# Performance work log

Measured on AMD Instinct MI355X. Metric: run time of the kernel, lower is better.

The kernel has to match this reference:

```python
import jax, jax.numpy as jnp
import numpy as np

B, C, H, W = 4, 64, 64, 64
RC, RS = 8, 4  # channel reduction, spatial reduction
CR = C // RC
KS = 2 * RS - 1  # 7


def _conv(x, w, b, stride, pad):
    y = jax.lax.conv_general_dilated(
        x, w, (stride, stride), [(pad, pad), (pad, pad)],
        dimension_numbers=('NCHW', 'OIHW', 'NCHW'))
    return y + b[None, :, None, None]


def setup_inputs() -> dict:
    key = jax.random.key(0)
    ks = jax.random.split(key, 13)

    def w_init(k, shape):
        fan_in = shape[1] * shape[2] * shape[3]
        return jax.random.normal(k, shape, jnp.float32) / jnp.sqrt(fan_in)

    x = jax.random.normal(ks[0], (B, C, H, W), jnp.float32)
    return {
        'x': x,
        'w1': w_init(ks[1], (CR, C, 1, 1)), 'b1': jnp.zeros((CR,), jnp.float32),
        'w2': w_init(ks[2], (CR, C, 1, 1)), 'b2': jnp.zeros((CR,), jnp.float32),
        'w3': w_init(ks[3], (C, C, 1, 1)),  'b3': jnp.zeros((C,), jnp.float32),
        'w4': w_init(ks[4], (C, C, KS, KS)), 'b4': jnp.zeros((C,), jnp.float32),
        'w5': w_init(ks[5], (C, C, KS, KS)), 'b5': jnp.zeros((C,), jnp.float32),
        'w6': w_init(ks[6], (C, C, 1, 1)),  'b6': jnp.zeros((C,), jnp.float32),
    }


def reference(x, w1, b1, w2, b2, w3, b3, w4, b4, w5, b5, w6, b6):
    gamma = 1.0
    x_ori = x
    b, c, h, w = x.shape
    n = h * w

    # ---- Block 1: spatial self-attention (SAGAN-style), N x N scores ----
    f = _conv(x, w1, b1, 1, 0).reshape(b, CR, n)   # [B, C/8, N]
    g = _conv(x, w2, b2, 1, 0).reshape(b, CR, n)   # [B, C/8, N]
    hh = _conv(x, w3, b3, 1, 0).reshape(b, c, n)   # [B, C, N]
    s = jnp.einsum('bci,bcj->bij', f, g)           # [B, N, N] = f^T g
    beta = jax.nn.softmax(s, axis=1)               # softmax over dim 1 (as in torch)
    o = jnp.einsum('bcn,bnm->bcm', hh, beta)       # [B, C, N]
    x2 = o.reshape(b, c, h, w)

    # ---- Block 2: channel attention over strided-conv features, C x C scores ----
    hp, wp = h // RS, w // RS
    npix = hp * wp
    f2 = _conv(x2, w4, b4, RS, RS - 1).reshape(b, c, npix)  # [B, C, N']
    g2 = _conv(x2, w5, b5, RS, RS - 1).reshape(b, c, npix)  # [B, C, N']
    h2 = _conv(x2, w6, b6, 1, 0).reshape(b, c, n)           # [B, C, N]
    s2 = jnp.einsum('bcn,bdn->bcd', f2, g2)                 # [B, C, C] = f g^T
    beta2 = jax.nn.softmax(s2, axis=1)
    # o[b,d,n] = sum_c h2[b,c,n] * beta2[b,c,d]
    o2 = jnp.einsum('bcn,bcd->bdn', h2, beta2).reshape(b, c, h, w)

    return gamma * o2 + x_ori
```

## Files before the change

### kernel.cpp

```cpp
#include <hip/hip_runtime.h>
#include <math.h>

#define BB 4
#define CC 64
#define CRR 8
#define NN 4096

typedef __attribute__((ext_vector_type(8))) short bf16x8;
typedef __attribute__((ext_vector_type(4))) float f32x4;

__device__ inline float bf2f(ushort u) {
    union { uint i; float f; } v; v.i = (uint)u << 16; return v.f;
}
__device__ inline ushort f2bf(float f) {
    uint u = __builtin_bit_cast(uint, f);
    u = (u + 0x7FFFu + ((u >> 16) & 1u)) >> 16;
    return (ushort)u;
}
__device__ inline uint bfpack2(float a, float b) {
    uint ua = __builtin_bit_cast(uint, a);
    uint ub = __builtin_bit_cast(uint, b);
    ua = (ua + 0x7FFFu + ((ua >> 16) & 1u)) >> 16;
    ub = (ub + 0x7FFFu + ((ub >> 16) & 1u)) & 0xFFFF0000u;
    return ua | ub;
}
__device__ inline uint pkrtz(float a, float b) {
    return __builtin_amdgcn_perm(__builtin_bit_cast(uint, b),
                                 __builtin_bit_cast(uint, a), 0x07060302u);
}
__device__ inline float fexp2(float x) {
#if __has_builtin(__builtin_amdgcn_exp2f)
    return __builtin_amdgcn_exp2f(x);
#else
    float r; asm("v_exp_f32 %0, %1" : "=v"(r) : "v"(x)); return r;
#endif
}

#define X2P_B 313600

__global__ __launch_bounds__(256) void produce_fgh(
    const float* __restrict__ x,
    const float* __restrict__ w1, const float* __restrict__ b1,
    const float* __restrict__ w2, const float* __restrict__ b2,
    const float* __restrict__ w3, const float* __restrict__ b3,
    ushort* __restrict__ fT, ushort* __restrict__ gT, ushort* __restrict__ hhb)
{
    const float LOG2E = 1.4426950408889634f;
    int t = threadIdx.x;
    int b = blockIdx.x & 3;
    int n = ((blockIdx.x >> 2) << 6) + (t & 63);
    int og = __builtin_amdgcn_readfirstlane(t >> 6);

    const float* xb = x + ((size_t)b << 18) + n;
    float xv[64];
#pragma unroll
    for (int c = 0; c < 64; ++c) xv[c] = xb[(size_t)c << 12];

    if (og == 0) {
        ushort fo[8], go[8];
#pragma unroll
        for (int k = 0; k < 8; ++k) {
            float a1 = b1[k], a2 = b2[k];
#pragma unroll
            for (int c = 0; c < 64; ++c) {
                a1 = fmaf(w1[k * 64 + c], xv[c], a1);
                a2 = fmaf(w2[k * 64 + c], xv[c], a2);
            }
            fo[k] = f2bf(a1 * LOG2E); go[k] = f2bf(a2);
        }
        uint4 fq = make_uint4((uint)fo[0] | ((uint)fo[1] << 16),
                              (uint)fo[2] | ((uint)fo[3] << 16),
                              (uint)fo[4] | ((uint)fo[5] << 16),
                              (uint)fo[6] | ((uint)fo[7] << 16));
        uint4 gq = make_uint4((uint)go[0] | ((uint)go[1] << 16),
                              (uint)go[2] | ((uint)go[3] << 16),
                              (uint)go[4] | ((uint)go[5] << 16),
                              (uint)go[6] | ((uint)go[7] << 16));
        *(uint4*)&fT[((size_t)b << 15) + (size_t)n * 8] = fq;
        *(uint4*)&gT[((size_t)b << 15) + (size_t)n * 8] = gq;
#pragma unroll
        for (int k = 0; k < 4; ++k) {
            float a = b3[k];
#pragma unroll
            for (int c = 0; c < 64; ++c) a = fmaf(w3[k * 64 + c], xv[c], a);
            hhb[((size_t)b << 18) + ((size_t)k << 12) + n] = f2bf(a);
        }
    } else {
        int c0 = og * 20 - 16;
#pragma unroll
        for (int k = 0; k < 20; ++k) {
            float a = b3[c0 + k];
#pragma unroll
            for (int c = 0; c < 64; ++c) a = fmaf(w3[(c0 + k) * 64 + c], xv[c], a);
            hhb[((size_t)b << 18) + ((size_t)(c0 + k) << 12) + n] = f2bf(a);
        }
    }
}

__global__ __launch_bounds__(256) void wtz_kernel(
    const float* __restrict__ w4, const float* __restrict__ w5,
    const float* __restrict__ w6,
    ushort* __restrict__ Wt, ushort* __restrict__ w6b, ushort* __restrict__ x2p)
{
    int bid = blockIdx.x;
    int t = threadIdx.x;
    if (bid < 128) {
        int conv = bid >> 6, co = bid & 63;
        const float* W = conv ? w5 : w4;
        for (int i = t; i < 3136; i += 256) {
            int ci = i / 49, kk = i - ci * 49;
            Wt[(((size_t)(conv * 64 + co)) * 49 + kk) * 64 + ci] = f2bf(W[co * 3136 + i]);
        }
    } else if (bid == 128) {
#pragma unroll
        for (int k = 0; k < 16; ++k) {
            int i = k * 256 + t;
            w6b[i] = f2bf(w6[i]);
        }
    } else {
        int gid = (bid - 129) * 256 + t;
        if (gid >= 4 * 804) return;
        int b = gid / 804;
        int i = gid - b * 804;
        int py, px;
        if (i < 210) { py = i / 70; px = i - py * 70; }
        else if (i < 420) { int j = i - 210; int r = j / 70; py = 67 + r; px = j - r * 70; }
        else { int j = i - 420; int r = j / 6; py = 3 + r; int c = j - r * 6; px = c < 3 ? c : 64 + c; }
        ushort* p = x2p + (size_t)b * X2P_B + (size_t)(py * 70 + px) * 64;
        uint4 z = make_uint4(0, 0, 0, 0);
#pragma unroll
        for (int k = 0; k < 8; ++k) *(uint4*)(p + k * 8) = z;
    }
}

__global__ __launch_bounds__(1024) void attn_kernel(
    const ushort* __restrict__ fT, const ushort* __restrict__ gT,
    const ushort* __restrict__ hhb, const ushort* __restrict__ w6b,
    const float* __restrict__ b6,
    ushort* __restrict__ x2p, ushort* __restrict__ h2b)
{
    __shared__ __align__(16) char smem[98304];
    ushort* hhT = (ushort*)smem;
    ushort* PstB = (ushort*)(smem + 65536);
    float* Acc = (float*)smem;
    float* Lq  = (float*)(smem + 69632);
    ushort* x2s = (ushort*)(smem + 70656);

    int t = threadIdx.x;
    int q = t >> 8, tq = t & 255;
    int l = t & 63;
    int wq = tq >> 6;
    int w16 = t >> 6;
    int ml = l & 15, g = l >> 4;
    int b = blockIdx.x & 3;
    int mt = blockIdx.x >> 2;
    int m0 = mt << 6;
    int col = m0 + wq * 16 + ml;

    const ushort* fTb = fT + ((size_t)b << 15) + (size_t)q * 8192;
    const ushort* gTb = gT + ((size_t)b << 15);
    const ushort* hhB = hhb + ((size_t)b << 18) + (q << 10);

    const bf16x8 z8 = {0, 0, 0, 0, 0, 0, 0, 0};
    const f32x4 z4 = {0.f, 0.f, 0.f, 0.f};

    bf16x8 gfrag = *(const bf16x8*)(gTb + (size_t)col * 8);
    if (g != 0) gfrag = z8;

    int sc = tq >> 2, sp = tq & 3;
    const ushort* hrowBase = hhB + (size_t)sc * 4096 + sp * 16;
    int hdst = q * 8192 + sp * 1024 + sc * 8;

    uint4 h0 = *(const uint4*)(hrowBase);
    uint4 h1 = *(const uint4*)(hrowBase + 8);
    *(uint4*)&hhT[hdst] = h0;
    *(uint4*)&hhT[hdst + 512] = h1;
    bf16x8 afc[4];
#pragma unroll
    for (int s = 0; s < 4; ++s)
        afc[s] = *(const bf16x8*)(fTb + (size_t)(16 * s + ml) * 8);

    f32x4 acc[4] = {z4, z4, z4, z4};
    float rsum = 0.f;
    int swz = (ml & 7) << 4;
    char* pbase = (char*)PstB + w16 * 2048;
    __syncthreads();

    for (int nt = 0; nt < 16; ++nt) {
        int buf = nt & 1;
        bf16x8 afn[4];
        if (nt < 15) {
            int n0 = (nt + 1) << 6;
            h0 = *(const uint4*)(hrowBase + n0);
            h1 = *(const uint4*)(hrowBase + n0 + 8);
#pragma unroll
            for (int s = 0; s < 4; ++s)
                afn[s] = *(const bf16x8*)(fTb + (size_t)(n0 + 16 * s + ml) * 8);
        }

        f32x4 Sv[4];
#pragma unroll
        for (int s = 0; s < 4; ++s)
            Sv[s] = __builtin_amdgcn_mfma_f32_16x16x32_bf16(afc[s], gfrag, z4, 0, 0, 0);

        uint plo[4], phi[4];
#pragma unroll
        for (int s = 0; s < 4; ++s) {
            float p0 = fexp2(Sv[s][0]);
            float p1 = fexp2(Sv[s][1]);
            float p2 = fexp2(Sv[s][2]);
            float p3 = fexp2(Sv[s][3]);
            rsum += (p0 + p1) + (p2 + p3);
            plo[s] = pkrtz(p0, p1);
            phi[s] = pkrtz(p2, p3);
        }

#pragma unroll
        for (int s = 0; s < 4; ++s) {
            uint off = (uint)((ml * 128 + 32 * s + 8 * g) ^ swz);
            *(uint2*)(pbase + off) = make_uint2(plo[s], phi[s]);
        }

#pragma unroll
        for (int kk = 0; kk < 2; ++kk) {
            uint off = (uint)((ml * 128 + 64 * kk + 16 * g) ^ swz);
            bf16x8 pf = *(const bf16x8*)(pbase + off);
#pragma unroll
            for (int ct = 0; ct < 4; ++ct) {
                bf16x8 hf = *(const bf16x8*)&hhT[q * 8192 + buf * 4096 + (kk * 4 + g) * 512 + (16 * ct + ml) * 8];
                acc[ct] = __builtin_amdgcn_mfma_f32_16x16x32_bf16(hf, pf, acc[ct], 0, 0, 0);
            }
        }

        if (nt < 15) {
            int nb = (nt + 1) & 1;
            *(uint4*)&hhT[hdst + nb * 4096] = h0;
            *(uint4*)&hhT[hdst + nb * 4096 + 512] = h1;
#pragma unroll
            for (int s = 0; s < 4; ++s) afc[s] = afn[s];
        }
        __syncthreads();
    }

    rsum += __shfl_xor(rsum, 16);
    rsum += __shfl_xor(rsum, 32);

    {
        float* arow = Acc + q * 4352 + (wq * 16 + ml) * 68;
#pragma unroll
        for (int ct = 0; ct < 4; ++ct)
            *(f32x4*)(arow + 16 * ct + 4 * g) = acc[ct];
        if (g == 0) Lq[q * 64 + wq * 16 + ml] = rsum;
    }
    __syncthreads();

    {
        int m = t >> 4, c0 = (t & 15) << 2;
        float Ltot = Lq[m] + Lq[64 + m] + Lq[128 + m] + Lq[192 + m];
        float rL = 1.f / Ltot;
        f32x4 v0 = *(const f32x4*)(Acc + 0 * 4352 + m * 68 + c0);
        f32x4 v1 = *(const f32x4*)(Acc + 1 * 4352 + m * 68 + c0);
        f32x4 v2 = *(const f32x4*)(Acc + 2 * 4352 + m * 68 + c0);
        f32x4 v3 = *(const f32x4*)(Acc + 3 * 4352 + m * 68 + c0);
        f32x4 v;
#pragma unroll
        for (int r = 0; r < 4; ++r)
            v[r] = ((v0[r] + v1[r]) + (v2[r] + v3[r])) * rL;
        uint2 pk = make_uint2(bfpack2(v[0], v[1]), bfpack2(v[2], v[3]));
        int px = m + 3, py = mt + 3;
        *(uint2*)(x2p + (size_t)b * X2P_B + (size_t)(py * 70 + px) * 64 + c0) = pk;
        *(uint2*)(x2s + m * 72 + c0) = pk;
    }
    __syncthreads();

    {
        int dt = w16 & 3, mq = w16 >> 2;
        f32x4 hacc = z4;
#pragma unroll
        for (int kk = 0; kk < 2; ++kk) {
            bf16x8 xf = *(const bf16x8*)(x2s + (mq * 16 + ml) * 72 + 32 * kk + 8 * g);
            bf16x8 wf = *(const bf16x8*)(w6b + (size_t)(16 * dt + ml) * 64 + 32 * kk + 8 * g);
            hacc = __builtin_amdgcn_mfma_f32_16x16x32_bf16(wf, xf, hacc, 0, 0, 0);
        }
        ushort* h2row = h2b + ((size_t)b << 18) + (m0 + mq * 16 + ml);
#pragma unroll
        for (int r = 0; r < 4; ++r) {
            int d = 16 * dt + 4 * g + r;
            h2row[(size_t)d << 12] = f2bf(hacc[r] + b6[d]);
        }
    }
}

__global__ __launch_bounds__(256) void conv7_split_kernel(
    const ushort* __restrict__ x2p, const ushort* __restrict__ Wt,
    float* __restrict__ part)
{
    int t = threadIdx.x;
    int l = t & 63, w = t >> 6;
    int ml = l & 15, g = l >> 4;
    int lb = (blockIdx.x & 7) * 28 + (blockIdx.x >> 3);
    int bc = lb / 28;
    int idx = (lb % 28) * 4 + w;
    int ky = idx >> 4;
    int ct = (idx >> 2) & 3;
    int og = idx & 3;
    int conv = bc & 1, b = bc >> 1;

    int co0 = ct * 16;
    const ushort* wb = Wt + (size_t)conv * 200704
                     + (size_t)(co0 + ml) * 3136 + (size_t)(ky * 7) * 64 + g * 8;
    const ushort* xbase = x2p + (size_t)b * X2P_B + g * 8;

    int pixoff[4];
#pragma unroll
    for (int s = 0; s < 4; ++s) {
        int opix = og * 64 + s * 16 + ml;
        int oy = opix >> 4, ox = opix & 15;
        pixoff[s] = ((oy * 4 + ky) * 70 + ox * 4) * 64;
    }

    const f32x4 z4 = {0.f, 0.f, 0.f, 0.f};
    f32x4 acc[4] = {z4, z4, z4, z4};

#pragma unroll
    for (int kx = 0; kx < 7; ++kx) {
#pragma unroll
        for (int ci0 = 0; ci0 < 64; ci0 += 32) {
            bf16x8 av = *(const bf16x8*)(wb + kx * 64 + ci0);
#pragma unroll
            for (int s = 0; s < 4; ++s) {
                bf16x8 bv = *(const bf16x8*)(xbase + pixoff[s] + kx * 64 + ci0);
                acc[s] = __builtin_amdgcn_mfma_f32_16x16x32_bf16(av, bv, acc[s], 0, 0, 0);
            }
        }
    }

    float* pb = part + (size_t)(ky * 8 + bc) * 16384;
#pragma unroll
    for (int s = 0; s < 4; ++s) {
        int opix = og * 64 + s * 16 + ml;
#pragma unroll
        for (int r = 0; r < 4; ++r) {
            int co = co0 + 4 * g + r;
            pb[co * 256 + opix] = acc[s][r];
        }
    }
}

__global__ __launch_bounds__(256) void conv7_reduce_kernel(
    const float* __restrict__ part, const float* __restrict__ b4,
    const float* __restrict__ b5, float* __restrict__ f2, float* __restrict__ g2)
{
    int idx = (blockIdx.x * 256 + threadIdx.x) * 4;
    int bc = idx >> 14;
    int co = (idx >> 8) & 63;
    int conv = bc & 1, b = bc >> 1;
    int sub = idx & 16383;
    float4 s = make_float4(0.f, 0.f, 0.f, 0.f);
#pragma unroll
    for (int ky = 0; ky < 7; ++ky) {
        float4 v = *(const float4*)&part[(size_t)(ky * 8 + bc) * 16384 + sub];
        s.x += v.x; s.y += v.y; s.z += v.z; s.w += v.w;
    }
    float bias = (conv ? b5 : b4)[co];
    s.x += bias; s.y += bias; s.z += bias; s.w += bias;
    float* y = conv ? g2 : f2;
    *(float4*)&y[(size_t)b * 16384 + sub] = s;
}

__global__ __launch_bounds__(1024) void s2_softmax_kernel(
    const float* __restrict__ f2, const float* __restrict__ g2,
    float* __restrict__ beta2)
{
    __shared__ __align__(16) float g2t[4][64][68];
    __shared__ __align__(16) float s2f[64][68];
    __shared__ float red[6][64];
    int t = threadIdx.x;
    int b = blockIdx.x;
    int q = t >> 8, tq = t & 255;
    int nb = q * 64;

    {
        int n = tq & 63, c0 = tq >> 6;
#pragma unroll
        for (int k = 0; k < 16; ++k) {
            int cc = c0 * 16 + k;
            g2t[q][n][cc] = g2[((size_t)(b * 64 + cc) << 8) + nb + n];
        }
    }
    __syncthreads();

    int c = tq & 63, dq = tq >> 6, d0 = dq * 16;
    float acc[16];
#pragma unroll
    for (int k = 0; k < 16; ++k) acc[k] = 0.f;
    const float* frow = f2 + ((size_t)(b * 64 + c) << 8) + nb;
#pragma unroll 4
    for (int n = 0; n < 64; ++n) {
        float fv = frow[n];
#pragma unroll
        for (int jj = 0; jj < 4; ++jj) {
            float4 gv = *(const float4*)&g2t[q][n][d0 + jj * 4];
            acc[jj * 4 + 0] = fmaf(fv, gv.x, acc[jj * 4 + 0]);
            acc[jj * 4 + 1] = fmaf(fv, gv.y, acc[jj * 4 + 1]);
            acc[jj * 4 + 2] = fmaf(fv, gv.z, acc[jj * 4 + 2]);
            acc[jj * 4 + 3] = fmaf(fv, gv.w, acc[jj * 4 + 3]);
        }
    }
    __syncthreads();
    float* part = &g2t[0][0][0];
#pragma unroll
    for (int k = 0; k < 16; ++k) part[q * 4096 + c * 64 + d0 + k] = acc[k];
    __syncthreads();
    {
        int idx = t * 4;
        int cc = idx >> 6, dd = idx & 63;
        float4 s0 = *(const float4*)&part[cc * 64 + dd];
        float4 s1 = *(const float4*)&part[4096 + cc * 64 + dd];
        float4 s2v = *(const float4*)&part[8192 + cc * 64 + dd];
        float4 s3 = *(const float4*)&part[12288 + cc * 64 + dd];
        float4 s;
        s.x = (s0.x + s1.x) + (s2v.x + s3.x);
        s.y = (s0.y + s1.y) + (s2v.y + s3.y);
        s.z = (s0.z + s1.z) + (s2v.z + s3.z);
        s.w = (s0.w + s1.w) + (s2v.w + s3.w);
        *(float4*)&s2f[cc][dd] = s;
    }
    __syncthreads();
    if (t < 256) {
        int d = t & 63, cq = t >> 6;
        float mx = -3e38f;
#pragma unroll
        for (int k = 0; k < 16; ++k) mx = fmaxf(mx, s2f[cq * 16 + k][d]);
        red[cq][d] = mx;
    }
    __syncthreads();
    if (t < 64)
        red[4][t] = fmaxf(fmaxf(red[0][t], red[1][t]), fmaxf(red[2][t], red[3][t]));
    __syncthreads();
    if (t < 256) {
        int d = t & 63, cq = t >> 6;
        float mx = red[4][d];
        float s = 0.f;
#pragma unroll
        for (int k = 0; k < 16; ++k) s += __expf(s2f[cq * 16 + k][d] - mx);
        red[cq][d] = s;
    }
    __syncthreads();
    if (t < 64)
        red[5][t] = 1.f / ((red[0][t] + red[1][t]) + (red[2][t] + red[3][t]));
    __syncthreads();
    if (t < 256) {
        int d = t & 63, cq = t >> 6;
        float mx = red[4][d], r = red[5][d];
#pragma unroll
        for (int k = 0; k < 16; ++k) {
            int cc = cq * 16 + k;
            beta2[((size_t)b << 12) + cc * 64 + d] = __expf(s2f[cc][d] - mx) * r;
        }
    }
}

__global__ __launch_bounds__(256) void o2_residual_kernel(
    const ushort* __restrict__ h2b, const float* __restrict__ beta2,
    const float* __restrict__ x, float* __restrict__ out)
{
    __shared__ __align__(16) float b2s[64][64];
    __shared__ float h2s[64][65];
    int t = threadIdx.x;
    int b = blockIdx.x & 3;
    int n0 = (blockIdx.x >> 2) << 6;

    {
#pragma unroll
        for (int k = 0; k < 16; ++k) {
            int idx = k * 256 + t;
            b2s[idx >> 6][idx & 63] = beta2[((size_t)b << 12) + idx];
        }
        int n = t & 63; int c0 = t >> 6;
#pragma unroll
        for (int k = 0; k < 16; ++k) {
            int cc = c0 * 16 + k;
            h2s[cc][n] = bf2f(h2b[((size_t)(b * 64 + cc) << 12) + n0 + n]);
        }
    }
    __syncthreads();

    int n = t & 63, dg = t >> 6, d0 = dg * 16;
    float acc[16];
#pragma unroll
    for (int k = 0; k < 16; ++k) acc[k] = 0.f;

    for (int cc = 0; cc < 64; ++cc) {
        float hv = h2s[cc][n];
#pragma unroll
        for (int jj = 0; jj < 4; ++jj) {
            float4 bv = *reinterpret_cast<const float4*>(&b2s[cc][d0 + jj * 4]);
            acc[jj * 4 + 0] = fmaf(hv, bv.x, acc[jj * 4 + 0]);
            acc[jj * 4 + 1] = fmaf(hv, bv.y, acc[jj * 4 + 1]);
            acc[jj * 4 + 2] = fmaf(hv, bv.z, acc[jj * 4 + 2]);
            acc[jj * 4 + 3] = fmaf(hv, bv.w, acc[jj * 4 + 3]);
        }
    }
#pragma unroll
    for (int k = 0; k < 16; ++k) {
        int d = d0 + k;
        size_t o = ((size_t)(b * 64 + d) << 12) + n0 + n;
        out[o] = acc[k] + x[o];
    }
}

extern "C" void kernel_launch(void* const* d_in, const int* in_sizes, int n_in,
                              void* d_out, int out_size, void* d_ws, size_t ws_size,
                              hipStream_t stream)
{
    const float* x  = (const float*)d_in[0];
    const float* w1 = (const float*)d_in[1];
    const float* b1 = (const float*)d_in[2];
    const float* w2 = (const float*)d_in[3];
    const float* b2 = (const float*)d_in[4];
    const float* w3 = (const float*)d_in[5];
    const float* b3 = (const float*)d_in[6];
    const float* w4 = (const float*)d_in[7];
    const float* b4 = (const float*)d_in[8];
    const float* w5 = (const float*)d_in[9];
    const float* b5 = (const float*)d_in[10];
    const float* w6 = (const float*)d_in[11];
    const float* b6 = (const float*)d_in[12];
    float* out = (float*)d_out;

    ushort* u = (ushort*)d_ws;
    ushort* fT  = u;
    ushort* gT  = fT + 131072;
    ushort* hhb = gT + 131072;
    ushort* x2p = hhb + 1048576;
    ushort* h2b = x2p + 1254400;
    ushort* Wt  = h2b + 1048576;
    ushort* w6b = Wt + 401408;
    float* fr    = (float*)(w6b + 4096);
    float* f2    = fr;
    float* g2    = fr + 65536;
    float* beta2 = fr + 131072;
    float* part  = fr + 147456;

    produce_fgh<<<256, 256, 0, stream>>>(x, w1, b1, w2, b2, w3, b3, fT, gT, hhb);
    wtz_kernel<<<142, 256, 0, stream>>>(w4, w5, w6, Wt, w6b, x2p);
    attn_kernel<<<256, 1024, 0, stream>>>(fT, gT, hhb, w6b, b6, x2p, h2b);
    conv7_split_kernel<<<224, 256, 0, stream>>>(x2p, Wt, part);
    conv7_reduce_kernel<<<128, 256, 0, stream>>>(part, b4, b5, f2, g2);
    s2_softmax_kernel<<<BB, 1024, 0, stream>>>(f2, g2, beta2);
    o2_residual_kernel<<<256, 256, 0, stream>>>(h2b, beta2, x, out);
}
```

Measured before the change: 83.26 us.

## Pre-tile hh in MFMA fragment layout and read directly from global, drop LDS staging

The producer kernel now writes hh in a fragment-ready tiled layout (8 consecutive pixels per channel group), so the attention kernel can load MFMA B-operands straight from global/L2 instead of staging a transposed copy in LDS. This removes the LDS double-buffer, its stores, and the per-iteration __syncthreads in the main loop, and shrinks shared memory use. In exchange each wave issues more global loads per tile with no prefetch, so latency is exposed unless caches and occupancy hide it. The producer's hh stores become strided 2-byte scatters.

Result: slower. 86.77 us (+4.2%).

```diff
diff --git a/kernel.cpp b/kernel.cpp
--- a/kernel.cpp
+++ b/kernel.cpp
@@ -43,7 +43,7 @@
     const float* __restrict__ w1, const float* __restrict__ b1,
     const float* __restrict__ w2, const float* __restrict__ b2,
     const float* __restrict__ w3, const float* __restrict__ b3,
-    ushort* __restrict__ fT, ushort* __restrict__ gT, ushort* __restrict__ hhb)
+    ushort* __restrict__ fT, ushort* __restrict__ gT, ushort* __restrict__ hhf)
 {
     const float LOG2E = 1.4426950408889634f;
     int t = threadIdx.x;
@@ -55,6 +55,8 @@
     float xv[64];
 #pragma unroll
     for (int c = 0; c < 64; ++c) xv[c] = xb[(size_t)c << 12];
+
+    ushort* hn = hhf + ((size_t)b << 18) + ((size_t)(n >> 3) << 9) + (n & 7);
 
     if (og == 0) {
         ushort fo[8], go[8];
@@ -83,7 +85,7 @@
             float a = b3[k];
 #pragma unroll
             for (int c = 0; c < 64; ++c) a = fmaf(w3[k * 64 + c], xv[c], a);
-            hhb[((size_t)b << 18) + ((size_t)k << 12) + n] = f2bf(a);
+            hn[k << 3] = f2bf(a);
         }
     } else {
         int c0 = og * 20 - 16;
@@ -92,7 +94,7 @@
             float a = b3[c0 + k];
 #pragma unroll
             for (int c = 0; c < 64; ++c) a = fmaf(w3[(c0 + k) * 64 + c], xv[c], a);
-            hhb[((size_t)b << 18) + ((size_t)(c0 + k) << 12) + n] = f2bf(a);
+            hn[(c0 + k) << 3] = f2bf(a);
         }
     }
 }
@@ -135,13 +137,12 @@
 
 __global__ __launch_bounds__(1024) void attn_kernel(
     const ushort* __restrict__ fT, const ushort* __restrict__ gT,
-    const ushort* __restrict__ hhb, const ushort* __restrict__ w6b,
+    const ushort* __restrict__ hhf, const ushort* __restrict__ w6b,
     const float* __restrict__ b6,
     ushort* __restrict__ x2p, ushort* __restrict__ h2b)
 {
-    __shared__ __align__(16) char smem[98304];
-    ushort* hhT = (ushort*)smem;
-    ushort* PstB = (ushort*)(smem + 65536);
+    __shared__ __align__(16) char smem[79872];
+    ushort* PstB = (ushort*)smem;
     float* Acc = (float*)smem;
     float* Lq  = (float*)(smem + 69632);
     ushort* x2s = (ushort*)(smem + 70656);
@@ -159,7 +160,7 @@
 
     const ushort* fTb = fT + ((size_t)b << 15) + (size_t)q * 8192;
     const ushort* gTb = gT + ((size_t)b << 15);
-    const ushort* hhB = hhb + ((size_t)b << 18) + (q << 10);
+    const ushort* hhB = hhf + ((size_t)b << 18) + ((size_t)q << 16);
 
     const bf16x8 z8 = {0, 0, 0, 0, 0, 0, 0, 0};
     const f32x4 z4 = {0.f, 0.f, 0.f, 0.f};
@@ -167,14 +168,6 @@
     bf16x8 gfrag = *(const bf16x8*)(gTb + (size_t)col * 8);
     if (g != 0) gfrag = z8;
 
-    int sc = tq >> 2, sp = tq & 3;
-    const ushort* hrowBase = hhB + (size_t)sc * 4096 + sp * 16;
-    int hdst = q * 8192 + sp * 1024 + sc * 8;
-
-    uint4 h0 = *(const uint4*)(hrowBase);
-    uint4 h1 = *(const uint4*)(hrowBase + 8);
-    *(uint4*)&hhT[hdst] = h0;
-    *(uint4*)&hhT[hdst + 512] = h1;
     bf16x8 afc[4];
 #pragma unroll
     for (int s = 0; s < 4; ++s)
@@ -184,15 +177,11 @@
     float rsum = 0.f;
     int swz = (ml & 7) << 4;
     char* pbase = (char*)PstB + w16 * 2048;
-    __syncthreads();
 
     for (int nt = 0; nt < 16; ++nt) {
-        int buf = nt & 1;
         bf16x8 afn[4];
         if (nt < 15) {
             int n0 = (nt + 1) << 6;
-            h0 = *(const uint4*)(hrowBase + n0);
-            h1 = *(const uint4*)(hrowBase + n0 + 8);
 #pragma unroll
             for (int s = 0; s < 4; ++s)
                 afn[s] = *(const bf16x8*)(fTb + (size_t)(n0 + 16 * s + ml) * 8);
@@ -221,29 +210,28 @@
             *(uint2*)(pbase + off) = make_uint2(plo[s], phi[s]);
         }
 
+        const ushort* hnt = hhB + nt * 4096;
 #pragma unroll
         for (int kk = 0; kk < 2; ++kk) {
             uint off = (uint)((ml * 128 + 64 * kk + 16 * g) ^ swz);
             bf16x8 pf = *(const bf16x8*)(pbase + off);
 #pragma unroll
             for (int ct = 0; ct < 4; ++ct) {
-                bf16x8 hf = *(const bf16x8*)&hhT[q * 8192 + buf * 4096 + (kk * 4 + g) * 512 + (16 * ct + ml) * 8];
+                bf16x8 hf = *(const bf16x8*)(hnt + (kk * 4 + g) * 512 + (16 * ct + ml) * 8);
                 acc[ct] = __builtin_amdgcn_mfma_f32_16x16x32_bf16(hf, pf, acc[ct], 0, 0, 0);
             }
         }
 
         if (nt < 15) {
-            int nb = (nt + 1) & 1;
-            *(uint4*)&hhT[hdst + nb * 4096] = h0;
-            *(uint4*)&hhT[hdst + nb * 4096 + 512] = h1;
 #pragma unroll
             for (int s = 0; s < 4; ++s) afc[s] = afn[s];
         }
-        __syncthreads();
     }
 
     rsum += __shfl_xor(rsum, 16);
     rsum += __shfl_xor(rsum, 32);
+
+    __syncthreads();
 
     {
         float* arow = Acc + q * 4352 + (wq * 16 + ml) * 68;
@@ -532,8 +520,8 @@
     ushort* u = (ushort*)d_ws;
     ushort* fT  = u;
     ushort* gT  = fT + 131072;
-    ushort* hhb = gT + 131072;
-    ushort* x2p = hhb + 1048576;
+    ushort* hhf = gT + 131072;
+    ushort* x2p = hhf + 1048576;
     ushort* h2b = x2p + 1254400;
     ushort* Wt  = h2b + 1048576;
     ushort* w6b = Wt + 401408;
@@ -543,9 +531,9 @@
     float* beta2 = fr + 131072;
     float* part  = fr + 147456;
 
-    produce_fgh<<<256, 256, 0, stream>>>(x, w1, b1, w2, b2, w3, b3, fT, gT, hhb);
+    produce_fgh<<<256, 256, 0, stream>>>(x, w1, b1, w2, b2, w3, b3, fT, gT, hhf);
     wtz_kernel<<<142, 256, 0, stream>>>(w4, w5, w6, Wt, w6b, x2p);
-    attn_kernel<<<256, 1024, 0, stream>>>(fT, gT, hhb, w6b, b6, x2p, h2b);
+    attn_kernel<<<256, 1024, 0, stream>>>(fT, gT, hhf, w6b, b6, x2p, h2b);
     conv7_split_kernel<<<224, 256, 0, stream>>>(x2p, Wt, part);
     conv7_reduce_kernel<<<128, 256, 0, stream>>>(part, b4, b5, f2, g2);
     s2_softmax_kernel<<<BB, 1024, 0, stream>>>(f2, g2, beta2);
```

## Fuse strided 7x7 conv split-K partials and reduction into one kernel via LDS

Applied to the files above, without the earlier changes.

Merges the split-ky conv7 kernel and its separate reduction kernel into a single kernel. Each 448-thread block has seven waves, one per kernel row ky, computing 16 channels by 32 pixels. The partial sums are reduced through shared memory before bias is added and the result written. This removes a kernel launch and the global round trip of the partial buffer, at the cost of fewer MFMAs per wave and a block-wide barrier.

After: 79.80 us. -4.2%, faster.

```diff
diff --git a/kernel.cpp b/kernel.cpp
--- a/kernel.cpp
+++ b/kernel.cpp
@@ -291,19 +291,19 @@
     }
 }
 
-__global__ __launch_bounds__(256) void conv7_split_kernel(
+__global__ __launch_bounds__(448) void conv7_kernel(
     const ushort* __restrict__ x2p, const ushort* __restrict__ Wt,
-    float* __restrict__ part)
-{
+    const float* __restrict__ b4, const float* __restrict__ b5,
+    float* __restrict__ f2, float* __restrict__ g2)
+{
+    __shared__ float red[7][512];
     int t = threadIdx.x;
-    int l = t & 63, w = t >> 6;
+    int l = t & 63, ky = t >> 6;
     int ml = l & 15, g = l >> 4;
-    int lb = (blockIdx.x & 7) * 28 + (blockIdx.x >> 3);
-    int bc = lb / 28;
-    int idx = (lb % 28) * 4 + w;
-    int ky = idx >> 4;
-    int ct = (idx >> 2) & 3;
-    int og = idx & 3;
+    int bid = blockIdx.x;
+    int bc = bid & 7;
+    int sub = bid >> 3;
+    int ct = sub & 3, oh = sub >> 2;
     int conv = bc & 1, b = bc >> 1;
 
     int co0 = ct * 16;
@@ -311,16 +311,16 @@
                      + (size_t)(co0 + ml) * 3136 + (size_t)(ky * 7) * 64 + g * 8;
     const ushort* xbase = x2p + (size_t)b * X2P_B + g * 8;
 
-    int pixoff[4];
-#pragma unroll
-    for (int s = 0; s < 4; ++s) {
-        int opix = og * 64 + s * 16 + ml;
+    int pixoff[2];
+#pragma unroll
+    for (int s = 0; s < 2; ++s) {
+        int opix = oh * 32 + s * 16 + ml;
         int oy = opix >> 4, ox = opix & 15;
         pixoff[s] = ((oy * 4 + ky) * 70 + ox * 4) * 64;
     }
 
     const f32x4 z4 = {0.f, 0.f, 0.f, 0.f};
-    f32x4 acc[4] = {z4, z4, z4, z4};
+    f32x4 acc[2] = {z4, z4};
 
 #pragma unroll
     for (int kx = 0; kx < 7; ++kx) {
@@ -328,44 +328,30 @@
         for (int ci0 = 0; ci0 < 64; ci0 += 32) {
             bf16x8 av = *(const bf16x8*)(wb + kx * 64 + ci0);
 #pragma unroll
-            for (int s = 0; s < 4; ++s) {
+            for (int s = 0; s < 2; ++s) {
                 bf16x8 bv = *(const bf16x8*)(xbase + pixoff[s] + kx * 64 + ci0);
                 acc[s] = __builtin_amdgcn_mfma_f32_16x16x32_bf16(av, bv, acc[s], 0, 0, 0);
             }
         }
     }
 
-    float* pb = part + (size_t)(ky * 8 + bc) * 16384;
-#pragma unroll
-    for (int s = 0; s < 4; ++s) {
-        int opix = og * 64 + s * 16 + ml;
-#pragma unroll
-        for (int r = 0; r < 4; ++r) {
-            int co = co0 + 4 * g + r;
-            pb[co * 256 + opix] = acc[s][r];
-        }
-    }
-}
-
-__global__ __launch_bounds__(256) void conv7_reduce_kernel(
-    const float* __restrict__ part, const float* __restrict__ b4,
-    const float* __restrict__ b5, float* __restrict__ f2, float* __restrict__ g2)
-{
-    int idx = (blockIdx.x * 256 + threadIdx.x) * 4;
-    int bc = idx >> 14;
-    int co = (idx >> 8) & 63;
-    int conv = bc & 1, b = bc >> 1;
-    int sub = idx & 16383;
-    float4 s = make_float4(0.f, 0.f, 0.f, 0.f);
-#pragma unroll
-    for (int ky = 0; ky < 7; ++ky) {
-        float4 v = *(const float4*)&part[(size_t)(ky * 8 + bc) * 16384 + sub];
-        s.x += v.x; s.y += v.y; s.z += v.z; s.w += v.w;
-    }
-    float bias = (conv ? b5 : b4)[co];
-    s.x += bias; s.y += bias; s.z += bias; s.w += bias;
+#pragma unroll
+    for (int s = 0; s < 2; ++s)
+#pragma unroll
+        for (int r = 0; r < 4; ++r)
+            red[ky][(4 * g + r) * 32 + s * 16 + ml] = acc[s][r];
+    __syncthreads();
+
+    const float* bias = conv ? b5 : b4;
     float* y = conv ? g2 : f2;
-    *(float4*)&y[(size_t)b * 16384 + sub] = s;
+    for (int idx = t; idx < 512; idx += 448) {
+        float s = red[0][idx];
+        s += red[1][idx]; s += red[2][idx]; s += red[3][idx];
+        s += red[4][idx]; s += red[5][idx]; s += red[6][idx];
+        int co = co0 + (idx >> 5);
+        int opix = oh * 32 + (idx & 31);
+        y[((size_t)(b * 64 + co) << 8) + opix] = s + bias[co];
+    }
 }
 
 __global__ __launch_bounds__(1024) void s2_softmax_kernel(
@@ -541,13 +527,11 @@
     float* f2    = fr;
     float* g2    = fr + 65536;
     float* beta2 = fr + 131072;
-    float* part  = fr + 147456;
 
     produce_fgh<<<256, 256, 0, stream>>>(x, w1, b1, w2, b2, w3, b3, fT, gT, hhb);
     wtz_kernel<<<142, 256, 0, stream>>>(w4, w5, w6, Wt, w6b, x2p);
     attn_kernel<<<256, 1024, 0, stream>>>(fT, gT, hhb, w6b, b6, x2p, h2b);
-    conv7_split_kernel<<<224, 256, 0, stream>>>(x2p, Wt, part);
-    conv7_reduce_kernel<<<128, 256, 0, stream>>>(part, b4, b5, f2, g2);
+    conv7_kernel<<<256, 448, 0, stream>>>(x2p, Wt, b4, b5, f2, g2);
     s2_softmax_kernel<<<BB, 1024, 0, stream>>>(f2, g2, beta2);
     o2_residual_kernel<<<256, 256, 0, stream>>>(h2b, beta2, x, out);
 }
```
